# Kernel tuning notes

Hardware: AMD Instinct MI355X
Metric: run time of the kernel (lower is better)

## Reference

```python
import jax, jax.numpy as jnp
import numpy as np

LEVELS = 2
_H0 = jnp.array([0.0322231, -0.01260397, -0.09921954, 0.2978578,
                 0.80373875, 0.49761867, -0.02963553, -0.07576571], dtype=jnp.float32)
_H1 = _H0[::-1] * jnp.array([-1.0, 1.0] * 4, dtype=jnp.float32)  # db4 QMF


def subband_conv2d(x, kernel_2d, stride):
    # depthwise grouped conv: same 2D kernel applied to every channel
    C = x.shape[-1]
    k = jnp.tile(kernel_2d[:, :, None, None], (1, 1, 1, C))  # HWIO with I=1, groups=C
    return jax.lax.conv_general_dilated(
        x, k, window_strides=(stride, stride), padding='SAME',
        dimension_numbers=('NHWC', 'HWIO', 'NHWC'), feature_group_count=C)


def _upsample2d(t):
    B, H, W, C = t.shape
    return jnp.zeros((B, 2 * H, 2 * W, C), t.dtype).at[:, ::2, ::2, :].set(t)


def _local_conv(t, w):
    # per-spatial-position linear map over channels: [B,H,W,I] x [I,O,W,H] -> [B,H,W,O]
    return jnp.einsum('bhwi,iowh->bhwo', t, w)


def setup_inputs() -> dict:
    key = jax.random.key(0)
    ks = jax.random.split(key, 9)
    B, H, W, C, O = 16, 128, 128, 64, 64
    inp = {
        'x': jax.random.normal(ks[0], (B, H, W, C), dtype=jnp.float32),
        'wLL': 0.02 * jax.random.normal(ks[1], (C, O, 32, 32), dtype=jnp.float32),
        'wLH_l0': 0.02 * jax.random.normal(ks[2], (C, O, 64, 64), dtype=jnp.float32),
        'wHL_l0': 0.02 * jax.random.normal(ks[3], (C, O, 64, 64), dtype=jnp.float32),
        'wHH_l0': 0.02 * jax.random.normal(ks[4], (C, O, 64, 64), dtype=jnp.float32),
        'wLH_l1': 0.02 * jax.random.normal(ks[5], (C, O, 32, 32), dtype=jnp.float32),
        'wHL_l1': 0.02 * jax.random.normal(ks[6], (C, O, 32, 32), dtype=jnp.float32),
        'wHH_l1': 0.02 * jax.random.normal(ks[7], (C, O, 32, 32), dtype=jnp.float32),
    }
    return inp


def reference(x, wLL, wLH_l0, wHL_l0, wHH_l0, wLH_l1, wHL_l1, wHH_l1):
    h0, h1 = _H0, _H1
    g0, g1 = h0[::-1], h1[::-1]
    # H=W=128 is divisible by 2**levels, so no symmetric padding is needed.
    res = x
    details = []
    for _ in range(LEVELS):
        cLL = subband_conv2d(res, jnp.outer(h0, h0), 2)
        cLH = subband_conv2d(res, jnp.outer(h0, h1), 2)
        cHL = subband_conv2d(res, jnp.outer(h1, h0), 2)
        cHH = subband_conv2d(res, jnp.outer(h1, h1), 2)
        details.append((cLH, cHL, cHH))
        res = cLL
    yA = _local_conv(res, wLL)  # [B,32,32,O]
    det_w = [(wLH_l0, wHL_l0, wHH_l0), (wLH_l1, wHL_l1, wHH_l1)]
    td = []
    for i in range(LEVELS):
        lh, hl, hh = details[i]
        wlh, whl, whh = det_w[i]
        td.append((_local_conv(lh, wlh), _local_conv(hl, whl), _local_conv(hh, whh)))
    r = yA
    for i in reversed(range(LEVELS)):
        yLH, yHL, yHH = td[i]
        r = (subband_conv2d(_upsample2d(r), jnp.outer(g0, g0), 1)
             + subband_conv2d(_upsample2d(yLH), jnp.outer(g0, g1), 1)
             + subband_conv2d(_upsample2d(yHL), jnp.outer(g1, g0), 1)
             + subband_conv2d(_upsample2d(yHH), jnp.outer(g1, g1), 1))
    return r
```

## Files before the change

### kernel.cpp

```cpp
#include <hip/hip_runtime.h>

__device__ __constant__ float H0[8] = { 0.0322231f, -0.01260397f, -0.09921954f,  0.2978578f,
                                        0.80373875f, 0.49761867f, -0.02963553f, -0.07576571f};
__device__ __constant__ float H1[8] = { 0.07576571f, -0.02963553f, -0.49761867f, 0.80373875f,
                                       -0.2978578f, -0.09921954f,  0.01260397f,  0.0322231f};
__device__ __constant__ float G0[8] = {-0.07576571f, -0.02963553f,  0.49761867f, 0.80373875f,
                                        0.2978578f,  -0.09921954f, -0.01260397f, 0.0322231f};
__device__ __constant__ float G1[8] = { 0.0322231f,   0.01260397f, -0.09921954f, -0.2978578f,
                                        0.80373875f, -0.49761867f, -0.02963553f, 0.07576571f};

template<int HIN>
__global__ __launch_bounds__(256) void fwd_dwt(const float* __restrict__ in,
                                               float* __restrict__ oLL, float* __restrict__ oLH,
                                               float* __restrict__ oHL, float* __restrict__ oHH)
{
    constexpr int OH = HIN / 2;
    constexpr int TQ = OH / 2;
    const int tid = threadIdx.x;
    const int c = tid & 63;
    const int s = blockIdx.x * 4 + (tid >> 6);
    const int j = s % TQ;
    const int i = (s / TQ) % TQ;
    const int b = s / (TQ * TQ);

    float acc[2][2][4];
#pragma unroll
    for (int a = 0; a < 2; ++a)
#pragma unroll
        for (int d = 0; d < 2; ++d)
#pragma unroll
            for (int k = 0; k < 4; ++k) acc[a][d][k] = 0.f;

    const int iw0 = 4 * j - 3;
#pragma unroll
    for (int r = 0; r < 10; ++r) {
        const int ih = 4 * i + r - 3;
        if ((unsigned)ih < (unsigned)HIN) {
            const float* row = in + ((b * HIN + ih) * HIN) * 64 + c;
            float xv[10];
#pragma unroll
            for (int v = 0; v < 10; ++v) {
                const int iw = iw0 + v;
                xv[v] = ((unsigned)iw < (unsigned)HIN) ? row[iw * 64] : 0.f;
            }
            float h00 = 0.f, h01 = 0.f, h10 = 0.f, h11 = 0.f;
#pragma unroll
            for (int v = 0; v < 8; ++v) {
                h00 += H0[v] * xv[v];
                h10 += H1[v] * xv[v];
                h01 += H0[v] * xv[v + 2];
                h11 += H1[v] * xv[v + 2];
            }
#pragma unroll
            for (int ii = 0; ii < 2; ++ii) {
                const int u = r - 2 * ii;
                if (0 <= u && u < 8) {
                    const float a0 = H0[u], a1 = H1[u];
                    acc[ii][0][0] += a0 * h00;
                    acc[ii][0][1] += a0 * h10;
                    acc[ii][0][2] += a1 * h00;
                    acc[ii][0][3] += a1 * h10;
                    acc[ii][1][0] += a0 * h01;
                    acc[ii][1][1] += a0 * h11;
                    acc[ii][1][2] += a1 * h01;
                    acc[ii][1][3] += a1 * h11;
                }
            }
        }
    }

#pragma unroll
    for (int ii = 0; ii < 2; ++ii)
#pragma unroll
        for (int jj = 0; jj < 2; ++jj) {
            const int oh = 2 * i + ii, ow = 2 * j + jj;
            const int oidx = ((b * OH + oh) * OH + ow) * 64 + c;
            oLL[oidx] = acc[ii][jj][0];
            oLH[oidx] = acc[ii][jj][1];
            oHL[oidx] = acc[ii][jj][2];
            oHH[oidx] = acc[ii][jj][3];
        }
}

template<int HD>
__global__ __launch_bounds__(256) void act_tr(const float* __restrict__ in,
                                              float* __restrict__ outp)
{
    __shared__ float Ld[64][HD + 1];
    const int w = blockIdx.x;
    const int b = blockIdx.y;
    const int t = threadIdx.x;

    {
        const int i = t & 63;
        const int hq = t >> 6;
#pragma unroll
        for (int s = 0; s < HD / 4; ++s) {
            const int h = hq * (HD / 4) + s;
            Ld[i][h] = in[((size_t)(b * HD + h) * HD + w) * 64 + i];
        }
    }
    __syncthreads();
    {
        const int h = t & (HD - 1);
        const int iq = t / HD;
        constexpr int NIQ = 256 / HD;
#pragma unroll
        for (int s = 0; s < 64 / NIQ; ++s) {
            const int i = s * NIQ + iq;
            outp[((size_t)(w * 64 + i) * 16 + b) * HD + h] = Ld[i][h];
        }
    }
}

template<int HD, int WSL, int OT, int NBT>
__global__ __launch_bounds__(256) void local_conv_v10(
    const float* __restrict__ a0, const float* __restrict__ a1,
    const float* __restrict__ a2, const float* __restrict__ a3,
    const float* __restrict__ w0, const float* __restrict__ w1,
    const float* __restrict__ w2, const float* __restrict__ w3,
    float* __restrict__ o0, float* __restrict__ o1,
    float* __restrict__ o2, float* __restrict__ o3)
{
    constexpr int WH   = HD * HD;
    constexpr int OGN  = 64 / OT;
    constexpr int BGN  = 16 / NBT;
    constexpr int PERZ = (HD / WSL) * OGN * BGN;

    const int nwg = gridDim.x;
    const int hb  = blockIdx.x;
    const int l   = (hb & 7) * (nwg >> 3) + (hb >> 3);

    const int z  = l / PERZ;
    int rem      = l - z * PERZ;
    const int wq = rem / (OGN * BGN);
    rem         -= wq * (OGN * BGN);
    const int og = rem / BGN;
    const int bg = rem - og * BGN;

    const float* act = (z == 0) ? a0 : (z == 1) ? a1 : (z == 2) ? a2 : a3;
    const float* wgt = (z == 0) ? w0 : (z == 1) ? w1 : (z == 2) ? w2 : w3;
    float*       out = (z == 0) ? o0 : (z == 1) ? o1 : (z == 2) ? o2 : o3;

    const int t   = threadIdx.x;
    const int w_l = t / HD;
    const int hc  = t % HD;
    const int w   = wq * WSL + w_l;
    const int b0  = bg * NBT;
    const int o0g = og * OT;

    const float* wp = wgt + (size_t)o0g * WH + w * HD + hc;
    const float* ap = act + ((size_t)(w * 64) * 16 + b0) * HD + hc;

    float acc[NBT][OT];
#pragma unroll
    for (int j = 0; j < NBT; ++j)
#pragma unroll
        for (int q = 0; q < OT; ++q) acc[j][q] = 0.f;

    for (int ch = 0; ch < 32; ++ch) {
        const int i0 = ch * 2;
        float wr[2][OT];
        float ar[2][NBT];
#pragma unroll
        for (int ii = 0; ii < 2; ++ii) {
#pragma unroll
            for (int q = 0; q < OT; ++q)
                wr[ii][q] = wp[(size_t)((i0 + ii) * 64 + q) * WH];
#pragma unroll
            for (int j = 0; j < NBT; ++j)
                ar[ii][j] = ap[(size_t)((i0 + ii) * 16 + j) * HD];
        }
#pragma unroll
        for (int ii = 0; ii < 2; ++ii)
#pragma unroll
            for (int j = 0; j < NBT; ++j) {
                const float a = ar[ii][j];
#pragma unroll
                for (int q = 0; q < OT; ++q)
                    acc[j][q] += a * wr[ii][q];
            }
    }

#pragma unroll
    for (int j = 0; j < NBT; ++j) {
        const int b = b0 + j;
        float* op = out + ((size_t)(b * HD + hc) * HD + w) * 64 + o0g;
#pragma unroll
        for (int q4 = 0; q4 < OT / 4; ++q4) {
            float4 v = make_float4(acc[j][q4 * 4 + 0], acc[j][q4 * 4 + 1],
                                   acc[j][q4 * 4 + 2], acc[j][q4 * 4 + 3]);
            *(float4*)(op + q4 * 4) = v;
        }
    }
}

template<int HOUT>
__global__ __launch_bounds__(256) void inv_dwt(const float* __restrict__ yLL,
                                               const float* __restrict__ yLH,
                                               const float* __restrict__ yHL,
                                               const float* __restrict__ yHH,
                                               float* __restrict__ out)
{
    constexpr int HS = HOUT / 2;
    const int tid = threadIdx.x;
    const int c = tid & 63;
    const int s = blockIdx.x * 4 + (tid >> 6);
    const int j = s % HS;
    const int i = (s / HS) % HS;
    const int b = s / (HS * HS);

    float Pe[4] = {0.f, 0.f, 0.f, 0.f}, Po[4] = {0.f, 0.f, 0.f, 0.f};
    float Qe[4] = {0.f, 0.f, 0.f, 0.f}, Qo[4] = {0.f, 0.f, 0.f, 0.f};

#pragma unroll
    for (int ku = 0; ku < 4; ++ku) {
        const int m = i - 1 + ku;
        if ((unsigned)m < (unsigned)HS) {
            const float a0e = G0[1 + 2 * ku], a0o = G0[2 * ku];
            const float a1e = G1[1 + 2 * ku], a1o = G1[2 * ku];
            const int rowoff = (b * HS + m) * HS;
#pragma unroll
            for (int kv = 0; kv < 4; ++kv) {
                const int n = j - 1 + kv;
                if ((unsigned)n < (unsigned)HS) {
                    const int idx = (rowoff + n) * 64 + c;
                    const float yll = yLL[idx], ylh = yLH[idx];
                    const float yhl = yHL[idx], yhh = yHH[idx];
                    Pe[kv] += a0e * yll + a1e * yhl;
                    Po[kv] += a0o * yll + a1o * yhl;
                    Qe[kv] += a0e * ylh + a1e * yhh;
                    Qo[kv] += a0o * ylh + a1o * yhh;
                }
            }
        }
    }

    float o00 = 0.f, o01 = 0.f, o10 = 0.f, o11 = 0.f;
#pragma unroll
    for (int kv = 0; kv < 4; ++kv) {
        const float b0e = G0[1 + 2 * kv], b0o = G0[2 * kv];
        const float b1e = G1[1 + 2 * kv], b1o = G1[2 * kv];
        o00 += b0e * Pe[kv] + b1e * Qe[kv];
        o01 += b0o * Pe[kv] + b1o * Qe[kv];
        o10 += b0e * Po[kv] + b1e * Qo[kv];
        o11 += b0o * Po[kv] + b1o * Qo[kv];
    }

    const int h0 = 2 * i, w0 = 2 * j;
    const int base = ((b * HOUT + h0) * HOUT + w0) * 64 + c;
    out[base] = o00;
    out[base + 64] = o01;
    out[base + HOUT * 64] = o10;
    out[base + HOUT * 64 + 64] = o11;
}

extern "C" void kernel_launch(void* const* d_in, const int* in_sizes, int n_in,
                              void* d_out, int out_size, void* d_ws, size_t ws_size,
                              hipStream_t stream)
{
    const float* x    = (const float*)d_in[0];
    const float* wLL  = (const float*)d_in[1];
    const float* wLH0 = (const float*)d_in[2];
    const float* wHL0 = (const float*)d_in[3];
    const float* wHH0 = (const float*)d_in[4];
    const float* wLH1 = (const float*)d_in[5];
    const float* wHL1 = (const float*)d_in[6];
    const float* wHH1 = (const float*)d_in[7];
    float* out = (float*)d_out;
    float* ws  = (float*)d_ws;

    const int S0 = 16 * 64 * 64 * 64;
    const int S1 = 16 * 32 * 32 * 64;

    float* c0 = out;
    float* A0 = out;
    float* A1 = out + 3 * S0;

    float* c1 = ws;
    float* t0 = ws + 4 * S1;
    float* t1 = ws + 4 * S1 + 3 * S0;
    float* yA = ws + 7 * S1 + 3 * S0;
    float* r1 = ws;

    fwd_dwt<128><<<16 * 32 * 32 / 4, 256, 0, stream>>>(x, c0, c0 + S0, c0 + 2 * S0, c0 + 3 * S0);

    fwd_dwt<64><<<16 * 16 * 16 / 4, 256, 0, stream>>>(c0,
        c1 + 0 * S1, c1 + 1 * S1, c1 + 2 * S1, c1 + 3 * S1);

    act_tr<64><<<dim3(64, 16), 256, 0, stream>>>(c0 + 1 * S0, A0 + 0 * S0);
    act_tr<64><<<dim3(64, 16), 256, 0, stream>>>(c0 + 2 * S0, A0 + 1 * S0);
    act_tr<64><<<dim3(64, 16), 256, 0, stream>>>(c0 + 3 * S0, A0 + 2 * S0);

    act_tr<32><<<dim3(32, 16), 256, 0, stream>>>(c1 + 0 * S1, A1 + 0 * S1);
    act_tr<32><<<dim3(32, 16), 256, 0, stream>>>(c1 + 1 * S1, A1 + 1 * S1);
    act_tr<32><<<dim3(32, 16), 256, 0, stream>>>(c1 + 2 * S1, A1 + 2 * S1);
    act_tr<32><<<dim3(32, 16), 256, 0, stream>>>(c1 + 3 * S1, A1 + 3 * S1);

    local_conv_v10<64, 4, 8, 8><<<768, 256, 0, stream>>>(
        A0 + 0 * S0, A0 + 1 * S0, A0 + 2 * S0, nullptr,
        wLH0, wHL0, wHH0, nullptr,
        t0 + 0 * S0, t0 + 1 * S0, t0 + 2 * S0, nullptr);

    local_conv_v10<32, 8, 8, 4><<<512, 256, 0, stream>>>(
        A1 + 1 * S1, A1 + 2 * S1, A1 + 3 * S1, A1 + 0 * S1,
        wLH1, wHL1, wHH1, wLL,
        t1 + 0 * S1, t1 + 1 * S1, t1 + 2 * S1, yA);

    inv_dwt<64><<<16 * 32 * 32 / 4, 256, 0, stream>>>(
        yA, t1 + 0 * S1, t1 + 1 * S1, t1 + 2 * S1, r1);

    inv_dwt<128><<<16 * 64 * 64 / 4, 256, 0, stream>>>(
        r1, t0 + 0 * S0, t0 + 1 * S0, t0 + 2 * S0, out);
}
```

Measured before the change: 307.3 us.

## Merge both local-conv launches into one grid, batch transposes, double-buffer loads

Both local-conv kernels now run in a single launch of 2048 workgroups, dispatched by block index, and the four level-1 activation transposes are batched into one launch using a z grid dimension. The level-0 conv tile drops from 8 to 4 batches per thread, which doubles its workgroup count to 1536. The inner channel loop is software-pipelined with two register buffer sets so the next channel pair's loads are issued before the current FMAs. The goal is to cut launch overhead and tail idle time between small kernels and to hide global load latency. In exchange it uses more registers, and the smaller per-thread tile lowers weight reuse on level 0.

```diff
diff --git a/kernel.cpp b/kernel.cpp
--- a/kernel.cpp
+++ b/kernel.cpp
@@ -113,8 +113,45 @@
     }
 }
 
+template<int HD>
+__global__ __launch_bounds__(256) void act_tr4(
+    const float* __restrict__ s0, const float* __restrict__ s1,
+    const float* __restrict__ s2, const float* __restrict__ s3,
+    float* __restrict__ d0, float* __restrict__ d1,
+    float* __restrict__ d2, float* __restrict__ d3)
+{
+    __shared__ float Ld[64][HD + 1];
+    const int z = blockIdx.z;
+    const float* in  = (z == 0) ? s0 : (z == 1) ? s1 : (z == 2) ? s2 : s3;
+    float*       outp = (z == 0) ? d0 : (z == 1) ? d1 : (z == 2) ? d2 : d3;
+    const int w = blockIdx.x;
+    const int b = blockIdx.y;
+    const int t = threadIdx.x;
+
+    {
+        const int i = t & 63;
+        const int hq = t >> 6;
+#pragma unroll
+        for (int s = 0; s < HD / 4; ++s) {
+            const int h = hq * (HD / 4) + s;
+            Ld[i][h] = in[((size_t)(b * HD + h) * HD + w) * 64 + i];
+        }
+    }
+    __syncthreads();
+    {
+        const int h = t & (HD - 1);
+        const int iq = t / HD;
+        constexpr int NIQ = 256 / HD;
+#pragma unroll
+        for (int s = 0; s < 64 / NIQ; ++s) {
+            const int i = s * NIQ + iq;
+            outp[((size_t)(w * 64 + i) * 16 + b) * HD + h] = Ld[i][h];
+        }
+    }
+}
+
 template<int HD, int WSL, int OT, int NBT>
-__global__ __launch_bounds__(256) void local_conv_v10(
+__device__ __forceinline__ void lc_body(int l,
     const float* __restrict__ a0, const float* __restrict__ a1,
     const float* __restrict__ a2, const float* __restrict__ a3,
     const float* __restrict__ w0, const float* __restrict__ w1,
@@ -127,10 +164,6 @@
     constexpr int BGN  = 16 / NBT;
     constexpr int PERZ = (HD / WSL) * OGN * BGN;
 
-    const int nwg = gridDim.x;
-    const int hb  = blockIdx.x;
-    const int l   = (hb & 7) * (nwg >> 3) + (hb >> 3);
-
     const int z  = l / PERZ;
     int rem      = l - z * PERZ;
     const int wq = rem / (OGN * BGN);
@@ -158,29 +191,45 @@
 #pragma unroll
         for (int q = 0; q < OT; ++q) acc[j][q] = 0.f;
 
-    for (int ch = 0; ch < 32; ++ch) {
-        const int i0 = ch * 2;
-        float wr[2][OT];
-        float ar[2][NBT];
-#pragma unroll
-        for (int ii = 0; ii < 2; ++ii) {
-#pragma unroll
-            for (int q = 0; q < OT; ++q)
-                wr[ii][q] = wp[(size_t)((i0 + ii) * 64 + q) * WH];
-#pragma unroll
-            for (int j = 0; j < NBT; ++j)
-                ar[ii][j] = ap[(size_t)((i0 + ii) * 16 + j) * HD];
-        }
-#pragma unroll
-        for (int ii = 0; ii < 2; ++ii)
-#pragma unroll
-            for (int j = 0; j < NBT; ++j) {
-                const float a = ar[ii][j];
-#pragma unroll
-                for (int q = 0; q < OT; ++q)
-                    acc[j][q] += a * wr[ii][q];
-            }
-    }
+    float wrA[2][OT], arA[2][NBT], wrB[2][OT], arB[2][NBT];
+
+#define LC_LOAD(WR, AR, CH)                                                    \
+    {                                                                          \
+        const int i0_ = (CH) * 2;                                              \
+        _Pragma("unroll")                                                      \
+        for (int ii = 0; ii < 2; ++ii) {                                       \
+            _Pragma("unroll")                                                  \
+            for (int q = 0; q < OT; ++q)                                       \
+                WR[ii][q] = wp[(size_t)((i0_ + ii) * 64 + q) * WH];            \
+            _Pragma("unroll")                                                  \
+            for (int j = 0; j < NBT; ++j)                                      \
+                AR[ii][j] = ap[(size_t)((i0_ + ii) * 16 + j) * HD];            \
+        }                                                                      \
+    }
+
+#define LC_FMA(WR, AR)                                                         \
+    {                                                                          \
+        _Pragma("unroll")                                                      \
+        for (int ii = 0; ii < 2; ++ii) {                                       \
+            _Pragma("unroll")                                                  \
+            for (int j = 0; j < NBT; ++j) {                                    \
+                const float a_ = AR[ii][j];                                    \
+                _Pragma("unroll")                                              \
+                for (int q = 0; q < OT; ++q)                                   \
+                    acc[j][q] += a_ * WR[ii][q];                               \
+            }                                                                  \
+        }                                                                      \
+    }
+
+    LC_LOAD(wrA, arA, 0);
+    for (int ch = 0; ch < 32; ch += 2) {
+        LC_LOAD(wrB, arB, ch + 1);
+        LC_FMA(wrA, arA);
+        if (ch + 2 < 32) LC_LOAD(wrA, arA, ch + 2);
+        LC_FMA(wrB, arB);
+    }
+#undef LC_LOAD
+#undef LC_FMA
 
 #pragma unroll
     for (int j = 0; j < NBT; ++j) {
@@ -192,6 +241,34 @@
                                    acc[j][q4 * 4 + 2], acc[j][q4 * 4 + 3]);
             *(float4*)(op + q4 * 4) = v;
         }
+    }
+}
+
+__global__ __launch_bounds__(256) void local_conv_all(
+    const float* __restrict__ a00, const float* __restrict__ a01, const float* __restrict__ a02,
+    const float* __restrict__ w00, const float* __restrict__ w01, const float* __restrict__ w02,
+    float* __restrict__ o00, float* __restrict__ o01, float* __restrict__ o02,
+    const float* __restrict__ a10, const float* __restrict__ a11,
+    const float* __restrict__ a12, const float* __restrict__ a13,
+    const float* __restrict__ w10, const float* __restrict__ w11,
+    const float* __restrict__ w12, const float* __restrict__ w13,
+    float* __restrict__ o10, float* __restrict__ o11,
+    float* __restrict__ o12, float* __restrict__ o13)
+{
+    const int nwg = gridDim.x;
+    const int hb  = blockIdx.x;
+    const int l   = (hb & 7) * (nwg >> 3) + (hb >> 3);
+
+    if (l < 1536) {
+        lc_body<64, 4, 8, 4>(l,
+            a00, a01, a02, nullptr,
+            w00, w01, w02, nullptr,
+            o00, o01, o02, nullptr);
+    } else {
+        lc_body<32, 8, 8, 4>(l - 1536,
+            a10, a11, a12, a13,
+            w10, w11, w12, w13,
+            o10, o11, o12, o13);
     }
 }
 
@@ -292,17 +369,14 @@
     act_tr<64><<<dim3(64, 16), 256, 0, stream>>>(c0 + 2 * S0, A0 + 1 * S0);
     act_tr<64><<<dim3(64, 16), 256, 0, stream>>>(c0 + 3 * S0, A0 + 2 * S0);
 
-    act_tr<32><<<dim3(32, 16), 256, 0, stream>>>(c1 + 0 * S1, A1 + 0 * S1);
-    act_tr<32><<<dim3(32, 16), 256, 0, stream>>>(c1 + 1 * S1, A1 + 1 * S1);
-    act_tr<32><<<dim3(32, 16), 256, 0, stream>>>(c1 + 2 * S1, A1 + 2 * S1);
-    act_tr<32><<<dim3(32, 16), 256, 0, stream>>>(c1 + 3 * S1, A1 + 3 * S1);
-
-    local_conv_v10<64, 4, 8, 8><<<768, 256, 0, stream>>>(
-        A0 + 0 * S0, A0 + 1 * S0, A0 + 2 * S0, nullptr,
-        wLH0, wHL0, wHH0, nullptr,
-        t0 + 0 * S0, t0 + 1 * S0, t0 + 2 * S0, nullptr);
-
-    local_conv_v10<32, 8, 8, 4><<<512, 256, 0, stream>>>(
+    act_tr4<32><<<dim3(32, 16, 4), 256, 0, stream>>>(
+        c1 + 0 * S1, c1 + 1 * S1, c1 + 2 * S1, c1 + 3 * S1,
+        A1 + 0 * S1, A1 + 1 * S1, A1 + 2 * S1, A1 + 3 * S1);
+
+    local_conv_all<<<2048, 256, 0, stream>>>(
+        A0 + 0 * S0, A0 + 1 * S0, A0 + 2 * S0,
+        wLH0, wHL0, wHH0,
+        t0 + 0 * S0, t0 + 1 * S0, t0 + 2 * S0,
         A1 + 1 * S1, A1 + 2 * S1, A1 + 3 * S1, A1 + 0 * S1,
         wLH1, wHL1, wHH1, wLL,
         t1 + 0 * S1, t1 + 1 * S1, t1 + 2 * S1, yA);
```

Result: slower. 320.4 us (+4.3%).
